# Performance work log

Hardware: AMD Instinct MI355X
Metric: run time of the kernel (lower is better)

The kernel has to match this reference:

```python
import jax, jax.numpy as jnp
import numpy as np


def setup_inputs() -> dict:
    key = jax.random.key(0)
    k1, k2 = jax.random.split(key)
    B, N, M, C = 4, 8192, 8192, 3
    ref = jax.random.normal(k1, (B, N, C), dtype=jnp.float32)
    query = jax.random.normal(k2, (B, M, C), dtype=jnp.float32)
    return {"ref": ref, "query": query, "k": 16}


def reference(ref, query, k):
    # ref:   [B, N, C] reference points
    # query: [B, M, C] query points
    # Squared Euclidean distances via ||q||^2 + ||r||^2 - 2 q.r  -> [B, M, N]
    q_sq = jnp.sum(query * query, axis=-1, keepdims=True)          # [B, M, 1]
    r_sq = jnp.sum(ref * ref, axis=-1)[:, None, :]                 # [B, 1, N]
    cross = jnp.einsum("bmc,bnc->bmn", query, ref)                 # [B, M, N]
    d2 = jnp.maximum(q_sq + r_sq - 2.0 * cross, 0.0)
    # k smallest distances, sorted ascending (knn_cuda convention)
    neg_topk, idx = jax.lax.top_k(-d2, k)                          # [B, M, k]
    dist = jnp.sqrt(-neg_topk)
    return dist, idx
```

## Files before the change

### kernel.cpp

```cpp
#include <hip/hip_runtime.h>


#define TPB 128
#define QPB 16
#define SPL 8
#define KK 16
#define TILE_PTS 512
#define CAP 16
#define TRIG 8

typedef unsigned long long u64k;

#define CE(x, i, j)                                   \
  {                                                   \
    u64k ki_ = x[i], kj_ = x[j];                      \
    bool c_ = kj_ < ki_;                              \
    x[i] = c_ ? kj_ : ki_;                            \
    x[j] = c_ ? ki_ : kj_;                            \
  }

__device__ __forceinline__ void sort16(u64k x[KK]) {
  CE(x,0,1) CE(x,2,3) CE(x,4,5) CE(x,6,7) CE(x,8,9) CE(x,10,11) CE(x,12,13) CE(x,14,15)
  CE(x,0,2) CE(x,1,3) CE(x,4,6) CE(x,5,7) CE(x,8,10) CE(x,9,11) CE(x,12,14) CE(x,13,15)
  CE(x,1,2) CE(x,5,6) CE(x,9,10) CE(x,13,14)
  CE(x,0,4) CE(x,1,5) CE(x,2,6) CE(x,3,7) CE(x,8,12) CE(x,9,13) CE(x,10,14) CE(x,11,15)
  CE(x,2,4) CE(x,3,5) CE(x,10,12) CE(x,11,13)
  CE(x,1,2) CE(x,3,4) CE(x,5,6) CE(x,9,10) CE(x,11,12) CE(x,13,14)
  CE(x,0,8) CE(x,1,9) CE(x,2,10) CE(x,3,11) CE(x,4,12) CE(x,5,13) CE(x,6,14) CE(x,7,15)
  CE(x,4,8) CE(x,5,9) CE(x,6,10) CE(x,7,11)
  CE(x,2,4) CE(x,3,5) CE(x,6,8) CE(x,7,9) CE(x,10,12) CE(x,11,13)
  CE(x,1,2) CE(x,3,4) CE(x,5,6) CE(x,7,8) CE(x,9,10) CE(x,11,12) CE(x,13,14)
}

__device__ __forceinline__ void mergeTop16(u64k a[KK], u64k e[KK]) {
#pragma unroll
  for (int i = 0; i < KK; ++i) {
    u64k bv = e[KK - 1 - i];
    if (bv < a[i]) a[i] = bv;
  }
  CE(a,0,8) CE(a,1,9) CE(a,2,10) CE(a,3,11) CE(a,4,12) CE(a,5,13) CE(a,6,14) CE(a,7,15)
  CE(a,0,4) CE(a,1,5) CE(a,2,6) CE(a,3,7) CE(a,8,12) CE(a,9,13) CE(a,10,14) CE(a,11,15)
  CE(a,0,2) CE(a,1,3) CE(a,4,6) CE(a,5,7) CE(a,8,10) CE(a,9,11) CE(a,12,14) CE(a,13,15)
  CE(a,0,1) CE(a,2,3) CE(a,4,5) CE(a,6,7) CE(a,8,9) CE(a,10,11) CE(a,12,13) CE(a,14,15)
}

__global__ __launch_bounds__(TPB, 4) void knn_topk_kernel(
    const float* __restrict__ ref, const float* __restrict__ query,
    float* __restrict__ dout, float* __restrict__ iout, int N, int M) {
#pragma clang fp contract(off)
  __shared__ float4 tile[TILE_PTS];
  __shared__ unsigned int sd[CAP * TPB];
  __shared__ unsigned short sg[CAP * TPB];

  const int tid = threadIdx.x;
  const int h = tid & (SPL - 1);
  const int qid = blockIdx.x * QPB + (tid >> 3);
  const int b = qid / M;

  const float* qp = query + (size_t)qid * 3;
  const float qx = qp[0], qy = qp[1], qz = qp[2];
  float q2 = (qx * qx + qz * qz) + qy * qy;

  u64k kl[KK];
  float T;
  int cnt = 0;

  const float* refb = ref + (size_t)b * N * 3;

  auto compact = [&]() {
    u64k e[KK];
#pragma unroll
    for (int s = 0; s < KK; ++s) {
      unsigned int db = sd[s * TPB + tid];
      unsigned int gi = sg[s * TPB + tid];
      u64k key = ((u64k)db << 32) | gi;
      e[s] = (s < cnt) ? key : ~0ull;
    }
    sort16(e);
    mergeTop16(kl, e);
    cnt = 0;
    float a15 = __uint_as_float((unsigned)(kl[KK - 1] >> 32));
    float m = fminf(a15, __shfl_xor(a15, 1));
    m = fminf(m, __shfl_xor(m, 2));
    T = fminf(m, __shfl_xor(m, 4));
  };

  const int ntiles = N / TILE_PTS;
  for (int t = 0; t < ntiles; ++t) {
    __syncthreads();
    {
      int pl = tid * 4;
      const float4* rp =
          (const float4*)(refb + (size_t)(t * TILE_PTS + pl) * 3);
      float4 f0 = rp[0], f1 = rp[1], f2 = rp[2];
      float x0 = f0.x, y0 = f0.y, z0 = f0.z;
      float x1 = f0.w, y1 = f1.x, z1 = f1.y;
      float x2 = f1.z, y2 = f1.w, z2 = f2.x;
      float x3 = f2.y, y3 = f2.z, z3 = f2.w;
      tile[pl + 0] = make_float4(x0, y0, z0, (x0 * x0 + z0 * z0) + y0 * y0);
      tile[pl + 1] = make_float4(x1, y1, z1, (x1 * x1 + z1 * z1) + y1 * y1);
      tile[pl + 2] = make_float4(x2, y2, z2, (x2 * x2 + z2 * z2) + y2 * y2);
      tile[pl + 3] = make_float4(x3, y3, z3, (x3 * x3 + z3 * z3) + y3 * y3);
    }
    __syncthreads();
    const int tbase = t * TILE_PTS;
    int g0 = 0;
    if (t == 0) {
#pragma unroll
      for (int n = 0; n < KK; ++n) {
        float4 p = tile[n * SPL + h];
        float cr = qx * p.x;
        cr = __builtin_fmaf(qy, p.y, cr);
        cr = __builtin_fmaf(qz, p.z, cr);
        float s2 = q2 + p.w;
        float d2 = __builtin_fmaf(-2.0f, cr, s2);
        float d2c = d2 < 0.f ? 0.f : d2;
        kl[n] = ((u64k)__float_as_uint(d2c) << 32) | (unsigned)(n * SPL + h);
      }
      sort16(kl);
      float a15 = __uint_as_float((unsigned)(kl[KK - 1] >> 32));
      float m = fminf(a15, __shfl_xor(a15, 1));
      m = fminf(m, __shfl_xor(m, 2));
      T = fminf(m, __shfl_xor(m, 4));
      g0 = 16;
    }
    for (int g = g0; g < TILE_PTS / SPL; g += 8) {
#pragma unroll
      for (int u = 0; u < 8; ++u) {
        const int loc = (g + u) * SPL + h;
        float4 p = tile[loc];
        float cr = qx * p.x;
        cr = __builtin_fmaf(qy, p.y, cr);
        cr = __builtin_fmaf(qz, p.z, cr);
        float s2 = q2 + p.w;
        float d2 = __builtin_fmaf(-2.0f, cr, s2);
        if (d2 <= T) {
          float d2c = d2 < 0.f ? 0.f : d2;
          sd[cnt * TPB + tid] = __float_as_uint(d2c);
          sg[cnt * TPB + tid] = (unsigned short)(tbase + loc);
          cnt++;
        }
      }
      if (__any(cnt >= TRIG)) compact();
    }
  }
  if (__any(cnt > 0)) compact();

#pragma unroll
  for (int d = 1; d < SPL; d <<= 1) {
    u64k r[KK];
#pragma unroll
    for (int s = 0; s < KK; ++s) r[s] = __shfl_xor(kl[s], d);
    mergeTop16(kl, r);
  }

  if (h == 0) {
    float* dq = dout + (size_t)qid * KK;
    float* iq = iout + (size_t)qid * KK;
    float dv[KK], iv[KK];
#pragma unroll
    for (int o = 0; o < KK; ++o) {
      dv[o] = sqrtf(__uint_as_float((unsigned)(kl[o] >> 32)));
      iv[o] = (float)(unsigned)(kl[o] & 0xffffffffu);
    }
    ((float4*)dq)[0] = make_float4(dv[0], dv[1], dv[2], dv[3]);
    ((float4*)dq)[1] = make_float4(dv[4], dv[5], dv[6], dv[7]);
    ((float4*)dq)[2] = make_float4(dv[8], dv[9], dv[10], dv[11]);
    ((float4*)dq)[3] = make_float4(dv[12], dv[13], dv[14], dv[15]);
    ((float4*)iq)[0] = make_float4(iv[0], iv[1], iv[2], iv[3]);
    ((float4*)iq)[1] = make_float4(iv[4], iv[5], iv[6], iv[7]);
    ((float4*)iq)[2] = make_float4(iv[8], iv[9], iv[10], iv[11]);
    ((float4*)iq)[3] = make_float4(iv[12], iv[13], iv[14], iv[15]);
  }
}

extern "C" void kernel_launch(void* const* d_in, const int* in_sizes, int n_in,
                              void* d_out, int out_size, void* d_ws, size_t ws_size,
                              hipStream_t stream) {
  const float* ref = (const float*)d_in[0];
  const float* query = (const float*)d_in[1];
  const int B = 4, C = 3;
  int N = in_sizes[0] / (B * C);
  int M = in_sizes[1] / (B * C);
  float* dout = (float*)d_out;
  float* iout = dout + (size_t)out_size / 2;
  int totalQ = B * M;
  int blocks = totalQ / QPB;
  knn_topk_kernel<<<blocks, TPB, 0, stream>>>(ref, query, dout, iout, N, M);
}
```

Baseline: 260.3 us.

## Store ref tile as swizzled SoA and evaluate distances with packed FP32

The reference tile moves from an AoS float4 array to four separate x/y/z/norm arrays, using an XOR-swizzled float4 layout to avoid LDS bank conflicts. Each lane now owns a contiguous 64-point slice of the tile instead of a strided one. Distances are computed two at a time with v_pk_mul/fma/add_f32 inline asm, halving the VALU count for the distance math. The trade-off is more complex indexing, and the different point-to-lane assignment changes the order candidates are inserted, which can affect how ties are broken.

After: 261.9 us. About the same (+0.6%).

```diff
diff --git a/kernel.cpp b/kernel.cpp
--- a/kernel.cpp
+++ b/kernel.cpp
@@ -10,6 +10,23 @@
 #define TRIG 8
 
 typedef unsigned long long u64k;
+typedef float f32x2 __attribute__((ext_vector_type(2)));
+
+__device__ __forceinline__ f32x2 pk_mul(f32x2 a, f32x2 b) {
+  f32x2 d;
+  asm("v_pk_mul_f32 %0, %1, %2" : "=v"(d) : "v"(a), "v"(b));
+  return d;
+}
+__device__ __forceinline__ f32x2 pk_fma(f32x2 a, f32x2 b, f32x2 c) {
+  f32x2 d;
+  asm("v_pk_fma_f32 %0, %1, %2, %3" : "=v"(d) : "v"(a), "v"(b), "v"(c));
+  return d;
+}
+__device__ __forceinline__ f32x2 pk_add(f32x2 a, f32x2 b) {
+  f32x2 d;
+  asm("v_pk_add_f32 %0, %1, %2" : "=v"(d) : "v"(a), "v"(b));
+  return d;
+}
 
 #define CE(x, i, j)                                   \
   {                                                   \
@@ -48,9 +65,14 @@
     const float* __restrict__ ref, const float* __restrict__ query,
     float* __restrict__ dout, float* __restrict__ iout, int N, int M) {
 #pragma clang fp contract(off)
-  __shared__ float4 tile[TILE_PTS];
+  __shared__ float tx[TILE_PTS], ty[TILE_PTS], tz[TILE_PTS], tw[TILE_PTS];
   __shared__ unsigned int sd[CAP * TPB];
   __shared__ unsigned short sg[CAP * TPB];
+
+  float4* tx4 = (float4*)tx;
+  float4* ty4 = (float4*)ty;
+  float4* tz4 = (float4*)tz;
+  float4* tw4 = (float4*)tw;
 
   const int tid = threadIdx.x;
   const int h = tid & (SPL - 1);
@@ -59,7 +81,9 @@
 
   const float* qp = query + (size_t)qid * 3;
   const float qx = qp[0], qy = qp[1], qz = qp[2];
-  float q2 = (qx * qx + qz * qz) + qy * qy;
+  const float q2 = (qx * qx + qz * qz) + qy * qy;
+  const f32x2 qxx = {qx, qx}, qyy = {qy, qy}, qzz = {qz, qz};
+  const f32x2 q22 = {q2, q2}, n22 = {-2.0f, -2.0f};
 
   u64k kl[KK];
   float T;
@@ -83,6 +107,37 @@
     float m = fminf(a15, __shfl_xor(a15, 1));
     m = fminf(m, __shfl_xor(m, 2));
     T = fminf(m, __shfl_xor(m, 4));
+  };
+
+  auto evalg = [&](int j, f32x2& d01, f32x2& d23) {
+    int ridx = (h << 4) + (j ^ h);
+    float4 xs = tx4[ridx];
+    float4 ys = ty4[ridx];
+    float4 zs = tz4[ridx];
+    float4 ws = tw4[ridx];
+    f32x2 x01 = {xs.x, xs.y}, x23 = {xs.z, xs.w};
+    f32x2 y01 = {ys.x, ys.y}, y23 = {ys.z, ys.w};
+    f32x2 z01 = {zs.x, zs.y}, z23 = {zs.z, zs.w};
+    f32x2 w01 = {ws.x, ws.y}, w23 = {ws.z, ws.w};
+    f32x2 cr01 = pk_mul(qxx, x01);
+    cr01 = pk_fma(qyy, y01, cr01);
+    cr01 = pk_fma(qzz, z01, cr01);
+    f32x2 s01 = pk_add(q22, w01);
+    d01 = pk_fma(n22, cr01, s01);
+    f32x2 cr23 = pk_mul(qxx, x23);
+    cr23 = pk_fma(qyy, y23, cr23);
+    cr23 = pk_fma(qzz, z23, cr23);
+    f32x2 s23 = pk_add(q22, w23);
+    d23 = pk_fma(n22, cr23, s23);
+  };
+
+  auto app = [&](float d2, int gi) {
+    if (d2 <= T) {
+      float d2c = d2 < 0.f ? 0.f : d2;
+      sd[cnt * TPB + tid] = __float_as_uint(d2c);
+      sg[cnt * TPB + tid] = (unsigned short)gi;
+      cnt++;
+    }
   };
 
   const int ntiles = N / TILE_PTS;
@@ -97,49 +152,58 @@
       float x1 = f0.w, y1 = f1.x, z1 = f1.y;
       float x2 = f1.z, y2 = f1.w, z2 = f2.x;
       float x3 = f2.y, y3 = f2.z, z3 = f2.w;
-      tile[pl + 0] = make_float4(x0, y0, z0, (x0 * x0 + z0 * z0) + y0 * y0);
-      tile[pl + 1] = make_float4(x1, y1, z1, (x1 * x1 + z1 * z1) + y1 * y1);
-      tile[pl + 2] = make_float4(x2, y2, z2, (x2 * x2 + z2 * z2) + y2 * y2);
-      tile[pl + 3] = make_float4(x3, y3, z3, (x3 * x3 + z3 * z3) + y3 * y3);
+      int widx = ((tid >> 4) << 4) + ((tid & 15) ^ (tid >> 4));
+      tx4[widx] = make_float4(x0, x1, x2, x3);
+      ty4[widx] = make_float4(y0, y1, y2, y3);
+      tz4[widx] = make_float4(z0, z1, z2, z3);
+      tw4[widx] = make_float4((x0 * x0 + z0 * z0) + y0 * y0,
+                              (x1 * x1 + z1 * z1) + y1 * y1,
+                              (x2 * x2 + z2 * z2) + y2 * y2,
+                              (x3 * x3 + z3 * z3) + y3 * y3);
     }
     __syncthreads();
     const int tbase = t * TILE_PTS;
-    int g0 = 0;
+    int j0 = 0;
     if (t == 0) {
 #pragma unroll
-      for (int n = 0; n < KK; ++n) {
-        float4 p = tile[n * SPL + h];
-        float cr = qx * p.x;
-        cr = __builtin_fmaf(qy, p.y, cr);
-        cr = __builtin_fmaf(qz, p.z, cr);
-        float s2 = q2 + p.w;
-        float d2 = __builtin_fmaf(-2.0f, cr, s2);
-        float d2c = d2 < 0.f ? 0.f : d2;
-        kl[n] = ((u64k)__float_as_uint(d2c) << 32) | (unsigned)(n * SPL + h);
+      for (int j = 0; j < 4; ++j) {
+        f32x2 d01, d23;
+        evalg(j, d01, d23);
+        int gb = (h << 6) + (j << 2);
+        float v0 = d01.x < 0.f ? 0.f : d01.x;
+        float v1 = d01.y < 0.f ? 0.f : d01.y;
+        float v2 = d23.x < 0.f ? 0.f : d23.x;
+        float v3 = d23.y < 0.f ? 0.f : d23.y;
+        kl[j * 4 + 0] = ((u64k)__float_as_uint(v0) << 32) | (unsigned)(gb + 0);
+        kl[j * 4 + 1] = ((u64k)__float_as_uint(v1) << 32) | (unsigned)(gb + 1);
+        kl[j * 4 + 2] = ((u64k)__float_as_uint(v2) << 32) | (unsigned)(gb + 2);
+        kl[j * 4 + 3] = ((u64k)__float_as_uint(v3) << 32) | (unsigned)(gb + 3);
       }
       sort16(kl);
       float a15 = __uint_as_float((unsigned)(kl[KK - 1] >> 32));
       float m = fminf(a15, __shfl_xor(a15, 1));
       m = fminf(m, __shfl_xor(m, 2));
       T = fminf(m, __shfl_xor(m, 4));
-      g0 = 16;
-    }
-    for (int g = g0; g < TILE_PTS / SPL; g += 8) {
-#pragma unroll
-      for (int u = 0; u < 8; ++u) {
-        const int loc = (g + u) * SPL + h;
-        float4 p = tile[loc];
-        float cr = qx * p.x;
-        cr = __builtin_fmaf(qy, p.y, cr);
-        cr = __builtin_fmaf(qz, p.z, cr);
-        float s2 = q2 + p.w;
-        float d2 = __builtin_fmaf(-2.0f, cr, s2);
-        if (d2 <= T) {
-          float d2c = d2 < 0.f ? 0.f : d2;
-          sd[cnt * TPB + tid] = __float_as_uint(d2c);
-          sg[cnt * TPB + tid] = (unsigned short)(tbase + loc);
-          cnt++;
-        }
+      j0 = 4;
+    }
+    for (int j = j0; j < TILE_PTS / SPL / 4; j += 2) {
+      {
+        f32x2 d01, d23;
+        evalg(j, d01, d23);
+        int gb = tbase + (h << 6) + (j << 2);
+        app(d01.x, gb + 0);
+        app(d01.y, gb + 1);
+        app(d23.x, gb + 2);
+        app(d23.y, gb + 3);
+      }
+      {
+        f32x2 d01, d23;
+        evalg(j + 1, d01, d23);
+        int gb = tbase + (h << 6) + ((j + 1) << 2);
+        app(d01.x, gb + 0);
+        app(d01.y, gb + 1);
+        app(d23.x, gb + 2);
+        app(d23.y, gb + 3);
       }
       if (__any(cnt >= TRIG)) compact();
     }
```
